# Optimization experiments

Hardware: AMD Instinct MI355X
Metric: run time of the kernel (lower is better)

Reference implementation:

```python
import jax, jax.numpy as jnp
import numpy as np

# ---- constants from the adaptive-LIF (ALIF) cell in the efficient_spiking_networks repo ----
B_J0 = 0.01     # baseline threshold
BETA = 1.8      # adaptation coupling
LENS = 0.5      # surrogate-gradient width
SCALE = 6.0
HIGHT = 0.15
GAMMA = 0.5

B, C, T, D = 512, 3, 500, 40
N, OUT = 256, 12


@jax.custom_vjp
def spike_fn(x):
    return (x > 0.0).astype(x.dtype)

def _spike_fwd(x):
    return spike_fn(x), x

def _spike_bwd(x, g):
    def gauss(v, mu, sigma):
        return jnp.exp(-((v - mu) ** 2) / (2.0 * sigma * sigma)) / (jnp.sqrt(2.0 * jnp.pi) * sigma)
    sur = GAMMA * (gauss(x, 0.0, LENS) * (1.0 + HIGHT)
                   - gauss(x, LENS, SCALE * LENS) * HIGHT
                   - gauss(x, -LENS, SCALE * LENS) * HIGHT)
    return (g * sur,)

spike_fn.defvjp(_spike_fwd, _spike_bwd)


def setup_inputs() -> dict:
    key = jax.random.key(0)
    ks = jax.random.split(key, 16)
    xav1 = float(np.sqrt(2.0 / (C * D + N)))
    xav3 = float(np.sqrt(2.0 / (N + OUT)))
    kai = float(np.sqrt(2.0 / N))
    return {
        'x': jax.random.normal(ks[0], (B, C, T, D), dtype=jnp.float32),
        'thr': jnp.array(0.05, dtype=jnp.float32),
        'W1': jax.random.normal(ks[1], (N, C * D), dtype=jnp.float32) * xav1,
        'b1': jnp.zeros((N,), dtype=jnp.float32),
        'W2_in': jax.random.normal(ks[2], (N, N), dtype=jnp.float32) * float(np.sqrt(1.0 / N)),
        'b2_in': jnp.zeros((N,), dtype=jnp.float32),
        'W2_rec': jax.random.normal(ks[3], (N, N), dtype=jnp.float32) * kai,
        'b2_rec': jnp.zeros((N,), dtype=jnp.float32),
        'W3': jax.random.normal(ks[4], (OUT, N), dtype=jnp.float32) * xav3,
        'b3': jnp.zeros((OUT,), dtype=jnp.float32),
        'tau_adp1': 200.0 + 50.0 * jax.random.normal(ks[5], (N,), dtype=jnp.float32),
        'tau_m1': 20.0 + 5.0 * jax.random.normal(ks[6], (N,), dtype=jnp.float32),
        'tau_adp2': 200.0 + 50.0 * jax.random.normal(ks[7], (N,), dtype=jnp.float32),
        'tau_m2': 20.0 + 5.0 * jax.random.normal(ks[8], (N,), dtype=jnp.float32),
        'tau_m3': 10.0 + 1.0 * jax.random.normal(ks[9], (OUT,), dtype=jnp.float32),
    }


def _alif(I, mem, spk, badp, alpha, rho):
    # adaptive threshold update with previous spike, then LIF membrane update
    badp = rho * badp + (1.0 - rho) * spk
    Bth = B_J0 + BETA * badp
    mem = alpha * mem + (1.0 - alpha) * I - Bth * spk
    s = spike_fn(mem - Bth)
    return mem, s, badp


def reference(x, thr, W1, b1, W2_in, b2_in, W2_rec, b2_rec, W3, b3,
              tau_adp1, tau_m1, tau_adp2, tau_m2, tau_m3):
    b, c, t, d = x.shape
    # ternary input spikification through surrogate step
    xs = spike_fn(x - thr) - spike_fn(-thr - x)          # [b,c,t,d] in {-1,0,1}
    xs = jnp.transpose(xs, (2, 0, 1, 3)).reshape(t, b, c * d)  # [t,b,c*d]

    alpha1 = jnp.exp(-1.0 / tau_m1)
    rho1 = jnp.exp(-1.0 / tau_adp1)
    alpha2 = jnp.exp(-1.0 / tau_m2)
    rho2 = jnp.exp(-1.0 / tau_adp2)
    alpha3 = jnp.exp(-1.0 / tau_m3)

    n = W1.shape[0]
    out = W3.shape[0]
    z = lambda m: jnp.zeros((b, m), dtype=x.dtype)
    carry0 = (z(n), z(n), jnp.full((b, n), B_J0, x.dtype),
              z(n), z(n), jnp.full((b, n), B_J0, x.dtype),
              z(out), z(out))

    def step(carry, x_t):
        m1, s1, a1, m2, s2, a2, m3, acc = carry
        i1 = x_t @ W1.T + b1
        m1, s1, a1 = _alif(i1, m1, s1, a1, alpha1, rho1)
        i2 = s1 @ W2_in.T + b2_in + s2 @ W2_rec.T + b2_rec
        m2, s2, a2 = _alif(i2, m2, s2, a2, alpha2, rho2)
        i3 = s2 @ W3.T + b3
        m3 = alpha3 * m3 + (1.0 - alpha3) * i3
        acc = acc + m3
        return (m1, s1, a1, m2, s2, a2, m3, acc), None

    carry, _ = jax.lax.scan(step, carry0, xs)
    acc = carry[-1]
    return jax.nn.log_softmax(acc / t, axis=1)
```

## Files before the change

### kernel.cpp

```cpp
#include <hip/hip_runtime.h>
#include <math.h>

#define B_   512
#define T_   500
#define C_   3
#define D_   40
#define CD_  120
#define N_   256
#define OUT_ 12
#define G_   16

typedef __attribute__((ext_vector_type(8))) short short8;
typedef __attribute__((ext_vector_type(4))) float f32x4;

#define W2IN_F  0
#define W2REC_F 65536
#define W1_F    131072
#define W3_F    163840

__device__ __forceinline__ unsigned short f2bf(float v) {
    unsigned x = __float_as_uint(v);
    unsigned r = (x + 0x7fffu + ((x >> 16) & 1u)) >> 16;
    return (unsigned short)r;
}

__global__ void prep_kernel(const float* __restrict__ W1, const float* __restrict__ W2i,
                            const float* __restrict__ W2r, const float* __restrict__ W3,
                            unsigned short* __restrict__ wsu) {
    int i = blockIdx.x * 256 + threadIdx.x;
    if (i < 131072) {
        int r = i & 65535;
        int j = r & 7, lane = (r >> 3) & 63, nt = (r >> 9) & 15, kt = r >> 13;
        int n = nt * 16 + (lane & 15);
        int k = kt * 32 + ((lane >> 4) << 3) + j;
        const float* W = (i < 65536) ? W2i : W2r;
        wsu[i] = f2bf(W[n * 256 + k]);
    } else if (i < 163840) {
        int r = i - 131072;
        int j = r & 7, lane = (r >> 3) & 63, nt = (r >> 9) & 15, kt = r >> 13;
        int n = nt * 16 + (lane & 15);
        int k = kt * 32 + ((lane >> 4) << 3) + j;
        wsu[i] = (k < CD_) ? f2bf(W1[n * CD_ + k]) : (unsigned short)0;
    } else {
        int r = i - 163840;
        int j = r & 7, lane = (r >> 3) & 63, kt = r >> 9;
        int o = lane & 15;
        int k = kt * 32 + ((lane >> 4) << 3) + j;
        wsu[i] = (o < OUT_) ? f2bf(W3[o * 256 + k]) : (unsigned short)0;
    }
}

__global__ __launch_bounds__(512, 2) void scan_kernel(
    const float* __restrict__ x, const float* __restrict__ thr_p,
    const float* __restrict__ b1, const float* __restrict__ b2i,
    const float* __restrict__ b2r, const float* __restrict__ b3,
    const float* __restrict__ tau_adp1, const float* __restrict__ tau_m1,
    const float* __restrict__ tau_adp2, const float* __restrict__ tau_m2,
    const float* __restrict__ tau_m3,
    const unsigned short* __restrict__ wsu, float* __restrict__ out) {

    __shared__ __align__(16) unsigned short w2in_lds[65536];
    __shared__ __align__(16) unsigned short s1A[4096];
    __shared__ __align__(16) unsigned short s2A[4096];
    __shared__ __align__(16) unsigned short xsA[4096];
    __shared__ __align__(16) unsigned short w3L[4096];

    const int tid  = threadIdx.x;
    const int wave = tid >> 6, lane = tid & 63;
    const int l15  = lane & 15, qd = lane >> 4;
    const int b0   = blockIdx.x * G_;
    const int nt0  = wave * 2, nt1 = nt0 + 1;

    {
        const short8* src = (const short8*)(wsu + W2IN_F);
        short8* dst = (short8*)w2in_lds;
        #pragma unroll
        for (int i = 0; i < 16; ++i) dst[tid + i * 512] = src[tid + i * 512];
        ((short8*)w3L)[tid] = ((const short8*)(wsu + W3_F))[tid];
    }
    {
        short8 z = {0, 0, 0, 0, 0, 0, 0, 0};
        ((short8*)s2A)[tid] = z;
        if (tid >= 480) {
            int idx = tid - 480, tp = idx >> 4, row = idx & 15;
            *(short8*)&xsA[((tp * 4 + 3) * 64 + 48 + row) * 8] = z;
        }
    }
    short8 w1b[2][4];
    #pragma unroll
    for (int i = 0; i < 2; ++i)
        #pragma unroll
        for (int kt = 0; kt < 4; ++kt)
            w1b[i][kt] = *(const short8*)&wsu[W1_F + ((kt * 16 + nt0 + i) * 64 + lane) * 8];
    short8 w2rb[2][8];
    #pragma unroll
    for (int i = 0; i < 2; ++i)
        #pragma unroll
        for (int kt = 0; kt < 8; ++kt)
            w2rb[i][kt] = *(const short8*)&wsu[W2REC_F + ((kt * 16 + nt0 + i) * 64 + lane) * 8];

    const float thrv = thr_p[0];
    float p_al1[2], p_rh1[2], p_b1[2], p_al2[2], p_rh2[2], p_b2[2];
    #pragma unroll
    for (int i = 0; i < 2; ++i) {
        int n = (nt0 + i) * 16 + l15;
        p_al1[i] = expf(-1.0f / tau_m1[n]);
        p_rh1[i] = expf(-1.0f / tau_adp1[n]);
        p_al2[i] = expf(-1.0f / tau_m2[n]);
        p_rh2[i] = expf(-1.0f / tau_adp2[n]);
        p_b1[i]  = b1[n];
        p_b2[i]  = b2i[n] + b2r[n];
    }
    const int oi = (l15 < OUT_) ? l15 : 0;
    const float p_al3 = expf(-1.0f / tau_m3[oi]);
    const float p_b3  = (l15 < OUT_) ? b3[l15] : 0.f;

    const bool stg = (tid < 480);
    int sc_t = 0, sc_off = 0;
    const float* px = x;
    if (stg) {
        sc_t = tid / 240; int srr = tid % 240;
        int row = srr / 15, oct = srr % 15, k0 = oct * 8;
        int c = k0 / D_, d = k0 % D_;
        px = x + ((size_t)(b0 + row) * C_ + c) * (size_t)(T_ * D_) + d;
        sc_off = ((sc_t * 4 + (k0 >> 5)) * 64 + ((k0 >> 3) & 3) * 16 + row) * 8;
    }

    float4 xr0 = {0,0,0,0}, xr1 = {0,0,0,0};
    if (stg) { const float* p = px + (size_t)sc_t * D_;
               xr0 = *(const float4*)p; xr1 = *(const float4*)(p + 4); }
    __syncthreads();

    if (stg) {
        float tf[8];
        *(float4*)&tf[0] = xr0; *(float4*)&tf[4] = xr1;
        __align__(16) unsigned short tu[8];
        #pragma unroll
        for (int j = 0; j < 8; ++j)
            tu[j] = ((tf[j] - thrv) > 0.f) ? (unsigned short)0x3F80
                  : (((-thrv - tf[j]) > 0.f) ? (unsigned short)0xBF80 : (unsigned short)0);
        *(short8*)&xsA[sc_off] = *(const short8*)tu;
    }
    __syncthreads();

    float i1c[2][2][4];
    #pragma unroll
    for (int tp = 0; tp < 2; ++tp) {
        f32x4 d0 = {0.f,0.f,0.f,0.f}, d1 = d0;
        #pragma unroll
        for (int kt = 0; kt < 4; ++kt) {
            short8 ax = *(const short8*)&xsA[((tp * 4 + kt) * 64 + lane) * 8];
            d0 = __builtin_amdgcn_mfma_f32_16x16x32_bf16(ax, w1b[0][kt], d0, 0, 0, 0);
            d1 = __builtin_amdgcn_mfma_f32_16x16x32_bf16(ax, w1b[1][kt], d1, 0, 0, 0);
        }
        #pragma unroll
        for (int r = 0; r < 4; ++r) { i1c[tp][0][r] = d0[r]; i1c[tp][1][r] = d1[r]; }
    }
    if (stg) { const float* p = px + (size_t)(2 + sc_t) * D_;
               xr0 = *(const float4*)p; xr1 = *(const float4*)(p + 4); }

    float m1s[8] = {0,0,0,0,0,0,0,0}, s1s[8] = {0,0,0,0,0,0,0,0}, a1s[8];
    float m2s[8] = {0,0,0,0,0,0,0,0}, s2s[8] = {0,0,0,0,0,0,0,0}, a2s[8];
    #pragma unroll
    for (int i = 0; i < 8; ++i) { a1s[i] = 0.01f; a2s[i] = 0.01f; }
    float m3v[4] = {0,0,0,0}, accv[4] = {0,0,0,0};
    float i2v[8];

    #pragma unroll 1
    for (int t = 0; t < T_; ++t) {
        {
            const int tp = t & 1;
            #pragma unroll
            for (int i = 0; i < 2; ++i) {
                const int nt = nt0 + i;
                const int koff = ((nt >> 1) * 64 + (((nt & 1) << 1) | (l15 >> 3)) * 16) * 8 + (l15 & 7);
                #pragma unroll
                for (int r = 0; r < 4; ++r) {
                    const int idx = i * 4 + r;
                    float I = p_b1[i] + i1c[tp][i][r];
                    a1s[idx] = p_rh1[i] * a1s[idx] + (1.f - p_rh1[i]) * s1s[idx];
                    float Bth = 0.01f + 1.8f * a1s[idx];
                    m1s[idx] = p_al1[i] * m1s[idx] + (1.f - p_al1[i]) * I - Bth * s1s[idx];
                    s1s[idx] = ((m1s[idx] - Bth) > 0.f) ? 1.f : 0.f;
                    s1A[koff + (qd * 4 + r) * 8] = (s1s[idx] > 0.5f) ? (unsigned short)0x3F80
                                                                     : (unsigned short)0;
                }
            }
        }
        __syncthreads();

        {
            f32x4 c0a = {0.f,0.f,0.f,0.f}, c0b = c0a, c1a = c0a, c1b = c0a, c3 = c0a;
            __builtin_amdgcn_s_setprio(1);
            #pragma unroll
            for (int kt = 0; kt < 8; ++kt) {
                short8 a1f = *(const short8*)&s1A[(kt * 64 + lane) * 8];
                short8 a2f = *(const short8*)&s2A[(kt * 64 + lane) * 8];
                short8 bi0 = *(const short8*)&w2in_lds[((kt * 16 + nt0) * 64 + lane) * 8];
                short8 bi1 = *(const short8*)&w2in_lds[((kt * 16 + nt1) * 64 + lane) * 8];
                if (kt & 1) {
                    c0b = __builtin_amdgcn_mfma_f32_16x16x32_bf16(a1f, bi0, c0b, 0, 0, 0);
                    c1b = __builtin_amdgcn_mfma_f32_16x16x32_bf16(a1f, bi1, c1b, 0, 0, 0);
                    c0b = __builtin_amdgcn_mfma_f32_16x16x32_bf16(a2f, w2rb[0][kt], c0b, 0, 0, 0);
                    c1b = __builtin_amdgcn_mfma_f32_16x16x32_bf16(a2f, w2rb[1][kt], c1b, 0, 0, 0);
                } else {
                    c0a = __builtin_amdgcn_mfma_f32_16x16x32_bf16(a1f, bi0, c0a, 0, 0, 0);
                    c1a = __builtin_amdgcn_mfma_f32_16x16x32_bf16(a1f, bi1, c1a, 0, 0, 0);
                    c0a = __builtin_amdgcn_mfma_f32_16x16x32_bf16(a2f, w2rb[0][kt], c0a, 0, 0, 0);
                    c1a = __builtin_amdgcn_mfma_f32_16x16x32_bf16(a2f, w2rb[1][kt], c1a, 0, 0, 0);
                }
                if (wave == 7) {
                    short8 w3f = *(const short8*)&w3L[(kt * 64 + lane) * 8];
                    c3 = __builtin_amdgcn_mfma_f32_16x16x32_bf16(a2f, w3f, c3, 0, 0, 0);
                }
            }
            __builtin_amdgcn_s_setprio(0);
            #pragma unroll
            for (int r = 0; r < 4; ++r) { i2v[r] = c0a[r] + c0b[r]; i2v[4 + r] = c1a[r] + c1b[r]; }
            if (wave == 7 && t > 0) {
                #pragma unroll
                for (int r = 0; r < 4; ++r) {
                    m3v[r] = p_al3 * m3v[r] + (1.f - p_al3) * (c3[r] + p_b3);
                    accv[r] += m3v[r];
                }
            }
            if ((t & 1) && t < T_ - 1) {
                #pragma unroll
                for (int tp = 0; tp < 2; ++tp) {
                    f32x4 d0 = {0.f,0.f,0.f,0.f}, d1 = d0;
                    #pragma unroll
                    for (int kt = 0; kt < 4; ++kt) {
                        short8 ax = *(const short8*)&xsA[((tp * 4 + kt) * 64 + lane) * 8];
                        d0 = __builtin_amdgcn_mfma_f32_16x16x32_bf16(ax, w1b[0][kt], d0, 0, 0, 0);
                        d1 = __builtin_amdgcn_mfma_f32_16x16x32_bf16(ax, w1b[1][kt], d1, 0, 0, 0);
                    }
                    #pragma unroll
                    for (int r = 0; r < 4; ++r) { i1c[tp][0][r] = d0[r]; i1c[tp][1][r] = d1[r]; }
                }
            }
        }
        __syncthreads();

        {
            #pragma unroll
            for (int i = 0; i < 2; ++i) {
                const int nt = nt0 + i;
                const int koff = ((nt >> 1) * 64 + (((nt & 1) << 1) | (l15 >> 3)) * 16) * 8 + (l15 & 7);
                #pragma unroll
                for (int r = 0; r < 4; ++r) {
                    const int idx = i * 4 + r;
                    float I = p_b2[i] + i2v[idx];
                    a2s[idx] = p_rh2[i] * a2s[idx] + (1.f - p_rh2[i]) * s2s[idx];
                    float Bth = 0.01f + 1.8f * a2s[idx];
                    m2s[idx] = p_al2[i] * m2s[idx] + (1.f - p_al2[i]) * I - Bth * s2s[idx];
                    s2s[idx] = ((m2s[idx] - Bth) > 0.f) ? 1.f : 0.f;
                    s2A[koff + (qd * 4 + r) * 8] = (s2s[idx] > 0.5f) ? (unsigned short)0x3F80
                                                                     : (unsigned short)0;
                }
            }
            if (!(t & 1) && t < T_ - 2 && stg) {
                float tf[8];
                *(float4*)&tf[0] = xr0; *(float4*)&tf[4] = xr1;
                __align__(16) unsigned short tu[8];
                #pragma unroll
                for (int j = 0; j < 8; ++j)
                    tu[j] = ((tf[j] - thrv) > 0.f) ? (unsigned short)0x3F80
                          : (((-thrv - tf[j]) > 0.f) ? (unsigned short)0xBF80 : (unsigned short)0);
                *(short8*)&xsA[sc_off] = *(const short8*)tu;
                if (t <= T_ - 6) {
                    const float* p = px + (size_t)(t + 4 + sc_t) * D_;
                    xr0 = *(const float4*)p; xr1 = *(const float4*)(p + 4);
                }
            }
        }
    }
    __syncthreads();

    if (wave == 7) {
        f32x4 c3 = {0.f,0.f,0.f,0.f};
        #pragma unroll
        for (int kt = 0; kt < 8; ++kt) {
            short8 a2f = *(const short8*)&s2A[(kt * 64 + lane) * 8];
            short8 w3f = *(const short8*)&w3L[(kt * 64 + lane) * 8];
            c3 = __builtin_amdgcn_mfma_f32_16x16x32_bf16(a2f, w3f, c3, 0, 0, 0);
        }
        #pragma unroll
        for (int r = 0; r < 4; ++r) {
            m3v[r] = p_al3 * m3v[r] + (1.f - p_al3) * (c3[r] + p_b3);
            accv[r] += m3v[r];
        }
        #pragma unroll
        for (int r = 0; r < 4; ++r) {
            float L = accv[r] / (float)T_;
            float mx = (l15 < OUT_) ? L : -1e30f;
            #pragma unroll
            for (int off = 1; off < 16; off <<= 1)
                mx = fmaxf(mx, __shfl_xor(mx, off, 16));
            float e = (l15 < OUT_) ? expf(L - mx) : 0.f;
            float se = e;
            #pragma unroll
            for (int off = 1; off < 16; off <<= 1)
                se += __shfl_xor(se, off, 16);
            if (l15 < OUT_)
                out[(size_t)(b0 + qd * 4 + r) * OUT_ + l15] = L - mx - logf(se);
        }
    }
}

extern "C" void kernel_launch(void* const* d_in, const int* in_sizes, int n_in,
                              void* d_out, int out_size, void* d_ws, size_t ws_size,
                              hipStream_t stream) {
    (void)in_sizes; (void)n_in; (void)out_size; (void)ws_size;
    const float* x        = (const float*)d_in[0];
    const float* thr      = (const float*)d_in[1];
    const float* W1       = (const float*)d_in[2];
    const float* b1       = (const float*)d_in[3];
    const float* W2_in    = (const float*)d_in[4];
    const float* b2_in    = (const float*)d_in[5];
    const float* W2_rec   = (const float*)d_in[6];
    const float* b2_rec   = (const float*)d_in[7];
    const float* W3       = (const float*)d_in[8];
    const float* b3       = (const float*)d_in[9];
    const float* tau_adp1 = (const float*)d_in[10];
    const float* tau_m1   = (const float*)d_in[11];
    const float* tau_adp2 = (const float*)d_in[12];
    const float* tau_m2   = (const float*)d_in[13];
    const float* tau_m3   = (const float*)d_in[14];
    unsigned short* wsu = (unsigned short*)d_ws;
    float* out = (float*)d_out;

    prep_kernel<<<656, 256, 0, stream>>>(W1, W2_in, W2_rec, W3, wsu);
    scan_kernel<<<B_ / G_, 512, 0, stream>>>(x, thr, b1, b2_in, b2_rec, b3,
                                             tau_adp1, tau_m1, tau_adp2, tau_m2,
                                             tau_m3, wsu, out);
}
```

Measured before the change: 1.619 ms.

## Keep W2_in in AGPRs and double-buffer spike tiles to drop a barrier

Each wave now holds its W2_in tiles in accumulator registers, loaded once from global memory, instead of re-reading them from LDS every timestep. The MFMAs use inline asm so they can take AGPR operands directly. The s1/s2 spike buffers are double-buffered by timestep parity, which lets one __syncthreads per step be removed. Launch bounds drop to one block per CU to free the registers this needs. The cost is heavy register pressure, hand-written s_nop hazard padding, and reliance on the parity buffering being race-free.

```diff
diff --git a/kernel.cpp b/kernel.cpp
--- a/kernel.cpp
+++ b/kernel.cpp
@@ -50,7 +50,7 @@
     }
 }
 
-__global__ __launch_bounds__(512, 2) void scan_kernel(
+__global__ __launch_bounds__(512, 1) void scan_kernel(
     const float* __restrict__ x, const float* __restrict__ thr_p,
     const float* __restrict__ b1, const float* __restrict__ b2i,
     const float* __restrict__ b2r, const float* __restrict__ b3,
@@ -59,9 +59,8 @@
     const float* __restrict__ tau_m3,
     const unsigned short* __restrict__ wsu, float* __restrict__ out) {
 
-    __shared__ __align__(16) unsigned short w2in_lds[65536];
-    __shared__ __align__(16) unsigned short s1A[4096];
-    __shared__ __align__(16) unsigned short s2A[4096];
+    __shared__ __align__(16) unsigned short s1A[8192];
+    __shared__ __align__(16) unsigned short s2A[8192];
     __shared__ __align__(16) unsigned short xsA[4096];
     __shared__ __align__(16) unsigned short w3L[4096];
 
@@ -72,15 +71,10 @@
     const int nt0  = wave * 2, nt1 = nt0 + 1;
 
     {
-        const short8* src = (const short8*)(wsu + W2IN_F);
-        short8* dst = (short8*)w2in_lds;
-        #pragma unroll
-        for (int i = 0; i < 16; ++i) dst[tid + i * 512] = src[tid + i * 512];
         ((short8*)w3L)[tid] = ((const short8*)(wsu + W3_F))[tid];
-    }
-    {
         short8 z = {0, 0, 0, 0, 0, 0, 0, 0};
         ((short8*)s2A)[tid] = z;
+        ((short8*)s2A)[tid + 512] = z;
         if (tid >= 480) {
             int idx = tid - 480, tp = idx >> 4, row = idx & 15;
             *(short8*)&xsA[((tp * 4 + 3) * 64 + 48 + row) * 8] = z;
@@ -92,12 +86,19 @@
         #pragma unroll
         for (int kt = 0; kt < 4; ++kt)
             w1b[i][kt] = *(const short8*)&wsu[W1_F + ((kt * 16 + nt0 + i) * 64 + lane) * 8];
-    short8 w2rb[2][8];
-    #pragma unroll
-    for (int i = 0; i < 2; ++i)
-        #pragma unroll
-        for (int kt = 0; kt < 8; ++kt)
-            w2rb[i][kt] = *(const short8*)&wsu[W2REC_F + ((kt * 16 + nt0 + i) * 64 + lane) * 8];
+
+    short8 w2ib0[8], w2ib1[8], w2rb0[8], w2rb1[8];
+    #pragma unroll
+    for (int kt = 0; kt < 8; ++kt) {
+        w2ib0[kt] = *(const short8*)&wsu[W2IN_F  + ((kt * 16 + nt0) * 64 + lane) * 8];
+        w2ib1[kt] = *(const short8*)&wsu[W2IN_F  + ((kt * 16 + nt1) * 64 + lane) * 8];
+        w2rb0[kt] = *(const short8*)&wsu[W2REC_F + ((kt * 16 + nt0) * 64 + lane) * 8];
+        w2rb1[kt] = *(const short8*)&wsu[W2REC_F + ((kt * 16 + nt1) * 64 + lane) * 8];
+    }
+    #pragma unroll
+    for (int kt = 0; kt < 8; ++kt)
+        asm volatile("" : "+a"(w2ib0[kt]), "+a"(w2ib1[kt]),
+                          "+a"(w2rb0[kt]), "+a"(w2rb1[kt]));
 
     const float thrv = thr_p[0];
     float p_al1[2], p_rh1[2], p_b1[2], p_al2[2], p_rh2[2], p_b2[2];
@@ -168,6 +169,9 @@
 
     #pragma unroll 1
     for (int t = 0; t < T_; ++t) {
+        const int bufc = (t & 1) * 4096;
+        const int bufp = ((t + 1) & 1) * 4096;
+
         {
             const int tp = t & 1;
             #pragma unroll
@@ -182,8 +186,8 @@
                     float Bth = 0.01f + 1.8f * a1s[idx];
                     m1s[idx] = p_al1[i] * m1s[idx] + (1.f - p_al1[i]) * I - Bth * s1s[idx];
                     s1s[idx] = ((m1s[idx] - Bth) > 0.f) ? 1.f : 0.f;
-                    s1A[koff + (qd * 4 + r) * 8] = (s1s[idx] > 0.5f) ? (unsigned short)0x3F80
-                                                                     : (unsigned short)0;
+                    s1A[bufc + koff + (qd * 4 + r) * 8] = (s1s[idx] > 0.5f) ? (unsigned short)0x3F80
+                                                                            : (unsigned short)0;
                 }
             }
         }
@@ -194,26 +198,34 @@
             __builtin_amdgcn_s_setprio(1);
             #pragma unroll
             for (int kt = 0; kt < 8; ++kt) {
-                short8 a1f = *(const short8*)&s1A[(kt * 64 + lane) * 8];
-                short8 a2f = *(const short8*)&s2A[(kt * 64 + lane) * 8];
-                short8 bi0 = *(const short8*)&w2in_lds[((kt * 16 + nt0) * 64 + lane) * 8];
-                short8 bi1 = *(const short8*)&w2in_lds[((kt * 16 + nt1) * 64 + lane) * 8];
+                short8 a1f = *(const short8*)&s1A[bufc + (kt * 64 + lane) * 8];
+                short8 a2f = *(const short8*)&s2A[bufp + (kt * 64 + lane) * 8];
                 if (kt & 1) {
-                    c0b = __builtin_amdgcn_mfma_f32_16x16x32_bf16(a1f, bi0, c0b, 0, 0, 0);
-                    c1b = __builtin_amdgcn_mfma_f32_16x16x32_bf16(a1f, bi1, c1b, 0, 0, 0);
-                    c0b = __builtin_amdgcn_mfma_f32_16x16x32_bf16(a2f, w2rb[0][kt], c0b, 0, 0, 0);
-                    c1b = __builtin_amdgcn_mfma_f32_16x16x32_bf16(a2f, w2rb[1][kt], c1b, 0, 0, 0);
+                    asm("v_mfma_f32_16x16x32_bf16 %0, %1, %2, %0"
+                        : "+v"(c0b) : "v"(a1f), "a"(w2ib0[kt]));
+                    asm("v_mfma_f32_16x16x32_bf16 %0, %1, %2, %0"
+                        : "+v"(c1b) : "v"(a1f), "a"(w2ib1[kt]));
+                    asm("v_mfma_f32_16x16x32_bf16 %0, %1, %2, %0"
+                        : "+v"(c0b) : "v"(a2f), "a"(w2rb0[kt]));
+                    asm("v_mfma_f32_16x16x32_bf16 %0, %1, %2, %0"
+                        : "+v"(c1b) : "v"(a2f), "a"(w2rb1[kt]));
                 } else {
-                    c0a = __builtin_amdgcn_mfma_f32_16x16x32_bf16(a1f, bi0, c0a, 0, 0, 0);
-                    c1a = __builtin_amdgcn_mfma_f32_16x16x32_bf16(a1f, bi1, c1a, 0, 0, 0);
-                    c0a = __builtin_amdgcn_mfma_f32_16x16x32_bf16(a2f, w2rb[0][kt], c0a, 0, 0, 0);
-                    c1a = __builtin_amdgcn_mfma_f32_16x16x32_bf16(a2f, w2rb[1][kt], c1a, 0, 0, 0);
+                    asm("v_mfma_f32_16x16x32_bf16 %0, %1, %2, %0"
+                        : "+v"(c0a) : "v"(a1f), "a"(w2ib0[kt]));
+                    asm("v_mfma_f32_16x16x32_bf16 %0, %1, %2, %0"
+                        : "+v"(c1a) : "v"(a1f), "a"(w2ib1[kt]));
+                    asm("v_mfma_f32_16x16x32_bf16 %0, %1, %2, %0"
+                        : "+v"(c0a) : "v"(a2f), "a"(w2rb0[kt]));
+                    asm("v_mfma_f32_16x16x32_bf16 %0, %1, %2, %0"
+                        : "+v"(c1a) : "v"(a2f), "a"(w2rb1[kt]));
                 }
                 if (wave == 7) {
                     short8 w3f = *(const short8*)&w3L[(kt * 64 + lane) * 8];
                     c3 = __builtin_amdgcn_mfma_f32_16x16x32_bf16(a2f, w3f, c3, 0, 0, 0);
                 }
             }
+            asm volatile("s_nop 7\n\ts_nop 7\n\ts_nop 7"
+                         : "+v"(c0a), "+v"(c0b), "+v"(c1a), "+v"(c1b));
             __builtin_amdgcn_s_setprio(0);
             #pragma unroll
             for (int r = 0; r < 4; ++r) { i2v[r] = c0a[r] + c0b[r]; i2v[4 + r] = c1a[r] + c1b[r]; }
@@ -239,7 +251,6 @@
                 }
             }
         }
-        __syncthreads();
 
         {
             #pragma unroll
@@ -254,8 +265,8 @@
                     float Bth = 0.01f + 1.8f * a2s[idx];
                     m2s[idx] = p_al2[i] * m2s[idx] + (1.f - p_al2[i]) * I - Bth * s2s[idx];
                     s2s[idx] = ((m2s[idx] - Bth) > 0.f) ? 1.f : 0.f;
-                    s2A[koff + (qd * 4 + r) * 8] = (s2s[idx] > 0.5f) ? (unsigned short)0x3F80
-                                                                     : (unsigned short)0;
+                    s2A[bufc + koff + (qd * 4 + r) * 8] = (s2s[idx] > 0.5f) ? (unsigned short)0x3F80
+                                                                            : (unsigned short)0;
                 }
             }
             if (!(t & 1) && t < T_ - 2 && stg) {
@@ -277,10 +288,11 @@
     __syncthreads();
 
     if (wave == 7) {
+        const int buff = ((T_ - 1) & 1) * 4096;
         f32x4 c3 = {0.f,0.f,0.f,0.f};
         #pragma unroll
         for (int kt = 0; kt < 8; ++kt) {
-            short8 a2f = *(const short8*)&s2A[(kt * 64 + lane) * 8];
+            short8 a2f = *(const short8*)&s2A[buff + (kt * 64 + lane) * 8];
             short8 w3f = *(const short8*)&w3L[(kt * 64 + lane) * 8];
             c3 = __builtin_amdgcn_mfma_f32_16x16x32_bf16(a2f, w3f, c3, 0, 0, 0);
         }
```

Measured after the change: 2.748 ms. 69.7% more time.
